# Kernel optimization log

Measured on AMD Instinct MI355X. Metric: run time of the kernel, lower is better.

The kernel has to match this reference:

```python
import jax, jax.numpy as jnp
import numpy as np

DIM = 384
HEADS = 8


def setup_inputs() -> dict:
    key = jax.random.key(0)
    ks = jax.random.split(key, 8)
    d = DIM
    return {
        "x": jax.random.normal(ks[0], (4, d, 128, 128), jnp.float32),
        "message": jax.random.normal(ks[1], (4, d, 128, 128), jnp.float32),
        "temperature": jnp.ones((HEADS, 1, 1), jnp.float32),
        "qkv_w": jax.random.normal(ks[2], (3 * d, d), jnp.float32) * 0.02,   # 1x1 conv weight
        "dw_w": jax.random.normal(ks[3], (3 * d, 1, 3, 3), jnp.float32) * 0.02,  # depthwise 3x3
        "proj_w": jax.random.normal(ks[4], (d, d), jnp.float32) * 0.02,     # project_out 1x1
        "lin_w": jax.random.normal(ks[5], (d, 2 * d), jnp.float32) * 0.02,  # nn.Linear weight [out,in]
        "lin_b": jnp.zeros((d,), jnp.float32),
    }


def _qkv_branch(t, qkv_w, dw_w):
    # 1x1 conv (pointwise) then depthwise 3x3, groups = 3*dim
    y = jnp.einsum('oc,bchw->bohw', qkv_w, t)
    y = jax.lax.conv_general_dilated(
        y, dw_w, window_strides=(1, 1), padding='SAME',
        dimension_numbers=('NCHW', 'OIHW', 'NCHW'),
        feature_group_count=dw_w.shape[0])
    return jnp.split(y, 3, axis=1)  # q, k, v each [b, dim, h, w]


def _to_heads(t):
    b, c, h, w = t.shape
    return t.reshape(b, HEADS, c // HEADS, h * w)  # [b, head, c, n]


def _l2norm(t):
    # torch F.normalize(dim=-1, eps=1e-12)
    n = jnp.sqrt(jnp.sum(t * t, axis=-1, keepdims=True))
    return t / jnp.maximum(n, 1e-12)


def reference(x, message, temperature, qkv_w, dw_w, proj_w, lin_w, lin_b):
    b, c, h, w = x.shape
    q, k, v = (_to_heads(t) for t in _qkv_branch(x, qkv_w, dw_w))
    q_m, k_m, v_m = (_to_heads(t) for t in _qkv_branch(message, qkv_w, dw_w))

    k_c = jnp.concatenate([k, k_m], axis=2)   # [b, head, 2c, n]
    v_c = jnp.concatenate([v, v_m], axis=2)

    q = _l2norm(q)
    k_c = _l2norm(k_c)
    q_m = _l2norm(q_m)

    # channel attention: [b, head, c, 2c]
    attn1 = jax.nn.softmax(jnp.einsum('bhcn,bhdn->bhcd', q, k_c) * temperature, axis=-1)
    attn2 = jax.nn.softmax(jnp.einsum('bhcn,bhdn->bhcd', q_m, k_c) * temperature, axis=-1)

    out1 = jnp.einsum('bhcd,bhdn->bhcn', attn1, v_c)  # [b, head, c, n]
    out2 = jnp.einsum('bhcd,bhdn->bhcn', attn2, v_c)

    # 'b head c (h w) -> b (h w) (head c)'
    out1 = out1.transpose(0, 3, 1, 2).reshape(b, h * w, c)
    out2 = out2.transpose(0, 3, 1, 2).reshape(b, h * w, c)

    cat = jnp.concatenate([out1, out2], axis=2)  # [b, n, 2c]
    out = cat @ lin_w.T + lin_b                  # [b, n, c]

    # 'b (h w) c -> b c h w'
    out = out.transpose(0, 2, 1).reshape(b, c, h, w)
    out = jnp.einsum('oc,bchw->bohw', proj_w, out)
    return out
```

## Files before the change

kernel.cpp:

```cpp
#include <hip/hip_runtime.h>

typedef unsigned short u16;
typedef unsigned int u32;

#define BATCH 4
#define CDIM 384
#define IMG 128
#define HW 16384
#define QKVC 1152
#define NHEADS 8
#define CHD 48
#define DD2 96
#define KFIN 768

typedef __attribute__((ext_vector_type(8))) short bf16x8;
typedef __attribute__((ext_vector_type(4))) float f32x4;

__device__ __forceinline__ u16 f2bf(float f){
  union { float f; u32 u; } v; v.f = f;
  u32 u = v.u;
  u32 r = (u + 0x7fffu + ((u >> 16) & 1u)) >> 16;
  return (u16)r;
}
__device__ __forceinline__ float bf2f(u16 h){
  union { u32 u; float f; } v; v.u = ((u32)h) << 16;
  return v.f;
}

#define OFF_QKVX  ((size_t)0)
#define OFF_QKVM  ((size_t)150994944)
#define OFF_T     ((size_t)301989888)
#define OFF_SSQ   ((size_t)339738624)
#define OFF_S     ((size_t)339775488)
#define OFF_ATTN  ((size_t)340955136)
#define OFF_AFINB ((size_t)342134784)
#define OFF_W2    ((size_t)344494080)
#define OFF_B2    ((size_t)345673728)
#define OFF_WB    ((size_t)345675264)

typedef __attribute__((address_space(1))) const u32 gas_u32;
typedef __attribute__((address_space(3))) u32 las_u32;
__device__ __forceinline__ void gl_lds16(const u16* g, u16* l){
  __builtin_amdgcn_global_load_lds((gas_u32*)g, (las_u32*)l, 16, 0, 0);
}

__device__ __forceinline__ u16* t_row(u16* T0, u16* qkvm, int par, int ch){
  if (par == 0) return T0 + (size_t)ch * HW;
  int bq = ch / 384;
  int rr = ch - bq * 384;
  return qkvm + ((size_t)bq * QKVC + 2 * CDIM + rr) * HW;
}

__global__ void __launch_bounds__(256) k_w2(const float* __restrict__ proj,
                                            const float* __restrict__ lin,
                                            const float* __restrict__ linb,
                                            const float* __restrict__ qkvw,
                                            float* __restrict__ W2,
                                            float* __restrict__ b2,
                                            u16* __restrict__ Wb){
  int idx = blockIdx.x * 256 + threadIdx.x;
  if (idx < CDIM * KFIN){
    int o = idx / KFIN, d = idx % KFIN;
    float acc = 0.f;
    for (int c = 0; c < CDIM; c++)
      acc = fmaf(proj[o * CDIM + c], lin[c * KFIN + d], acc);
    W2[idx] = acc;
  }
  if (idx < CDIM){
    float acc = 0.f;
    for (int c = 0; c < CDIM; c++)
      acc = fmaf(proj[idx * CDIM + c], linb[c], acc);
    b2[idx] = acc;
  }
  if (idx < QKVC * CDIM) Wb[idx] = f2bf(qkvw[idx]);
}

__device__ __forceinline__ void loadrow(const u16* __restrict__ src, int r, int cg, float* o){
  if ((unsigned)r >= IMG){
    #pragma unroll
    for (int i = 0; i < 18; i++) o[i] = 0.f;
    return;
  }
  const u16* p = src + (size_t)r * IMG + cg * 16;
  uint4 v0 = *(const uint4*)p;
  uint4 v1 = *(const uint4*)(p + 8);
  u32 ww[8] = {v0.x, v0.y, v0.z, v0.w, v1.x, v1.y, v1.z, v1.w};
  #pragma unroll
  for (int i = 0; i < 8; i++){
    union { u32 u; float f; } lo, hi;
    lo.u = ww[i] << 16;
    hi.u = ww[i] & 0xffff0000u;
    o[1 + 2 * i] = lo.f;
    o[2 + 2 * i] = hi.f;
  }
  o[0]  = (cg > 0) ? bf2f(p[-1]) : 0.f;
  o[17] = (cg < 7) ? bf2f(p[16]) : 0.f;
}

#define LCHUNK 1024
__global__ void __launch_bounds__(256) k_stage(
    int t, int npw, int nlog, int ndw, int ncvt,
    const u16* __restrict__ Wb, u16* __restrict__ Bt,
    u16* __restrict__ T0, u16* __restrict__ qkvx, u16* __restrict__ qkvm,
    const float* __restrict__ x, const float* __restrict__ msg,
    const float* __restrict__ dww, float* __restrict__ ssq,
    float* __restrict__ S){
  __shared__ __align__(16) u16 smem[16384];
  int bid = blockIdx.x;
  int tid = threadIdx.x;

  if (bid < npw){
    int z = t - 1, par = z & 1;
    const u16* B = Bt + (size_t)z * HW * CDIM;
    u16* As = smem;
    u16* Bs = smem + 8192;
    int swz = (bid & 7) * 144 + (bid >> 3);
    int bx = swz % 9, by = swz / 9;
    int m0 = bx * 128, n0 = by * 128;
    int w = tid >> 6, lane = tid & 63;
    int wy = w >> 1, wx = w & 1;
    int lm = lane & 15, q = lane >> 4;

    int srow = w * 16 + (lane >> 2);
    int scol = (lane & 3) * 8;
    const u16* ga = Wb + (size_t)(m0 + srow) * CDIM + scol;
    const u16* gb = B + (size_t)(n0 + srow) * CDIM + scol;
    u16* la = As + srow * 32 + scol;
    u16* lb = Bs + srow * 32 + scol;

    f32x4 acc[4][4];
    #pragma unroll
    for (int i = 0; i < 4; i++)
      #pragma unroll
      for (int j = 0; j < 4; j++) acc[i][j] = (f32x4){0.f,0.f,0.f,0.f};

#define PW_STAGE(buf, k0) do{ \
      gl_lds16(ga + (k0),             la + (buf) * 4096); \
      gl_lds16(ga + 64*CDIM + (k0),   la + (buf) * 4096 + 2048); \
      gl_lds16(gb + (k0),             lb + (buf) * 4096); \
      gl_lds16(gb + 64*CDIM + (k0),   lb + (buf) * 4096 + 2048); \
    }while(0)

    PW_STAGE(0, 0);
    __syncthreads();
    int cur = 0;
    for (int kt = 0; kt < 12; kt++){
      if (kt < 11) PW_STAGE(cur ^ 1, (kt + 1) * 32);
      bf16x8 af[4], bfr[4];
      #pragma unroll
      for (int i = 0; i < 4; i++)
        af[i] = *(const bf16x8*)&As[cur * 4096 + (wy * 64 + i * 16 + lm) * 32 + q * 8];
      #pragma unroll
      for (int j = 0; j < 4; j++)
        bfr[j] = *(const bf16x8*)&Bs[cur * 4096 + (wx * 64 + j * 16 + lm) * 32 + q * 8];
      #pragma unroll
      for (int i = 0; i < 4; i++)
        #pragma unroll
        for (int j = 0; j < 4; j++)
          acc[i][j] = __builtin_amdgcn_mfma_f32_16x16x32_bf16(af[i], bfr[j], acc[i][j], 0, 0, 0);
      __syncthreads();
      cur ^= 1;
    }
#undef PW_STAGE
    #pragma unroll
    for (int i = 0; i < 4; i++){
      #pragma unroll
      for (int r = 0; r < 4; r++){
        int row = m0 + wy * 64 + i * 16 + q * 4 + r;
        u16* cp = t_row(T0, qkvm, par, row) + n0 + wx * 64 + lm;
        #pragma unroll
        for (int j = 0; j < 4; j++)
          cp[j * 16] = f2bf(acc[i][j][r]);
      }
    }

  } else if (bid < npw + nlog){
    int idx = bid - npw;
    int b = t - 7;
    int nc = idx & 15;
    int h = idx >> 4;
    int w = tid >> 6, lane = tid & 63;
    int wy = w >> 1, wx = w & 1;
    int lm = lane & 15, quad = lane >> 4;

    const u16* ap[3]; const u16* bp[3];
    #pragma unroll
    for (int i = 0; i < 3; i++){
      int g = wy * 48 + i * 16 + lm;
      int c = (g < 48) ? g : g - 48;
      ap[i] = ((g < 48) ? qkvx : qkvm) + ((size_t)b * QKVC + h * CHD + c) * HW;
      int d = wx * 48 + i * 16 + lm;
      int cc = (d < 48) ? d : d - 48;
      bp[i] = ((d < 48) ? qkvx : qkvm) + ((size_t)b * QKVC + CDIM + h * CHD + cc) * HW;
    }
    f32x4 acc[3][3];
    #pragma unroll
    for (int i = 0; i < 3; i++)
      #pragma unroll
      for (int j = 0; j < 3; j++) acc[i][j] = (f32x4){0.f,0.f,0.f,0.f};

    int nbeg = nc * LCHUNK + quad * 8;
    int nend = nc * LCHUNK + LCHUNK;
    for (int n = nbeg; n < nend; n += 32){
      bf16x8 af[3], bfr[3];
      #pragma unroll
      for (int i = 0; i < 3; i++) af[i]  = *(const bf16x8*)(ap[i] + n);
      #pragma unroll
      for (int j = 0; j < 3; j++) bfr[j] = *(const bf16x8*)(bp[j] + n);
      #pragma unroll
      for (int i = 0; i < 3; i++)
        #pragma unroll
        for (int j = 0; j < 3; j++)
          acc[i][j] = __builtin_amdgcn_mfma_f32_16x16x32_bf16(af[i], bfr[j], acc[i][j], 0, 0, 0);
    }
    #pragma unroll
    for (int i = 0; i < 3; i++){
      #pragma unroll
      for (int r = 0; r < 4; r++){
        int g = wy * 48 + i * 16 + quad * 4 + r;
        int iq = (g >= 48) ? 1 : 0;
        int c = iq ? g - 48 : g;
        float* Sp = S + (((size_t)(iq * BATCH + b) * NHEADS + h) * CHD + c) * DD2;
        #pragma unroll
        for (int j = 0; j < 3; j++)
          atomicAdd(&Sp[wx * 48 + j * 16 + lm], acc[i][j][r]);
      }
    }

  } else if (bid < npw + nlog + ndw){
    int ch = bid - npw - nlog;
    int z = t - 2, par = z & 1;
    const u16* src = t_row(T0, qkvm, par, ch);
    u16* dst;
    if (ch < 2 * CDIM){
      u16* qd = ((z >> 2) ? qkvm : qkvx) + (size_t)(z & 3) * QKVC * HW;
      dst = qd + (size_t)ch * HW;
    } else {
      dst = Bt + (size_t)z * HW * CDIM + (size_t)(ch - 2 * CDIM) * HW;
    }
    float w[9];
    #pragma unroll
    for (int t9 = 0; t9 < 9; t9++) w[t9] = dww[ch * 9 + t9];
    int rg = tid >> 3, cg = tid & 7;
    int r0 = rg * 4;
    float ra[18], rb[18], rc[18];
    loadrow(src, r0 - 1, cg, ra);
    loadrow(src, r0,     cg, rb);
    float ss = 0.f;
    #pragma unroll
    for (int rr = 0; rr < 4; rr++){
      int r = r0 + rr;
      loadrow(src, r + 1, cg, rc);
      u32 pk[8];
      #pragma unroll
      for (int xx = 0; xx < 16; xx++){
        float a2 = w[0] * ra[xx];
        a2 = fmaf(w[1], ra[xx + 1], a2);
        a2 = fmaf(w[2], ra[xx + 2], a2);
        a2 = fmaf(w[3], rb[xx],     a2);
        a2 = fmaf(w[4], rb[xx + 1], a2);
        a2 = fmaf(w[5], rb[xx + 2], a2);
        a2 = fmaf(w[6], rc[xx],     a2);
        a2 = fmaf(w[7], rc[xx + 1], a2);
        a2 = fmaf(w[8], rc[xx + 2], a2);
        ss = fmaf(a2, a2, ss);
        u16 hv = f2bf(a2);
        if (xx & 1) pk[xx >> 1] |= (u32)hv << 16;
        else        pk[xx >> 1]  = (u32)hv;
      }
      *(uint4*)(dst + (size_t)r * IMG + cg * 16)     = *(uint4*)&pk[0];
      *(uint4*)(dst + (size_t)r * IMG + cg * 16 + 8) = *(uint4*)&pk[4];
      #pragma unroll
      for (int ii = 0; ii < 18; ii++){ ra[ii] = rb[ii]; rb[ii] = rc[ii]; }
    }
    if (ch < 2 * CDIM){
      float* red = (float*)smem;
      red[tid] = ss;
      __syncthreads();
      for (int s = 128; s > 0; s >>= 1){
        if (tid < s) red[tid] += red[tid + s];
        __syncthreads();
      }
      if (tid == 0) ssq[(size_t)z * QKVC + ch] = red[0];
    }

  } else if (bid < npw + nlog + ndw + ncvt){
    int cb = bid - npw - nlog - ndw;
    int z = t;
    const float* src = (z < 4 ? x : msg) + (size_t)(z & 3) * CDIM * HW;
    u16* dstz = Bt + (size_t)z * HW * CDIM;
    int n0 = (cb & 127) * 128;
    int c0 = (cb >> 7) * 64;
    u16 (*tile)[130] = (u16(*)[130])smem;
    #pragma unroll
    for (int i = 0; i < 8; i++){
      int c = (tid >> 5) + i * 8;
      int nq = tid & 31;
      float4 v = *(const float4*)(src + (size_t)(c0 + c) * HW + n0 + nq * 4);
      u32 p0 = (u32)f2bf(v.x) | ((u32)f2bf(v.y) << 16);
      u32 p1 = (u32)f2bf(v.z) | ((u32)f2bf(v.w) << 16);
      *(u32*)&tile[c][nq * 4]     = p0;
      *(u32*)&tile[c][nq * 4 + 2] = p1;
    }
    __syncthreads();
    #pragma unroll
    for (int u = 0; u < 2; u++){
      int idx = tid + u * 256;
      int n = idx >> 2, j = idx & 3;
      u32 pk[8];
      #pragma unroll
      for (int p = 0; p < 8; p++)
        pk[p] = (u32)tile[j * 16 + 2 * p][n] | ((u32)tile[j * 16 + 2 * p + 1][n] << 16);
      u16* dp = dstz + (size_t)(n0 + n) * CDIM + c0 + j * 16;
      *(uint4*)dp       = *(uint4*)&pk[0];
      *(uint4*)(dp + 8) = *(uint4*)&pk[4];
    }

  } else {
    int v = bid - npw - nlog - ndw - ncvt;
    int z, h, nb;
    if (v < 512){ z = t - 3; h = v >> 7; nb = v & 127; }
    else { int u = v - 512; z = u >> 9; h = 4 + ((u >> 7) & 3); nb = u & 127; }
    int inp = z >> 2, b = z & 3;
    const u16* vcn = Bt + (size_t)z * HW * CDIM;
    int n0 = nb * 128;
    u16* vt = (h < 4 ? qkvx : qkvm) + ((size_t)b * QKVC + 2 * CDIM) * HW;
    int dbase = (h & 3) * 96 + inp * 48;
    u16 (*tile)[136] = (u16(*)[136])smem;
    #pragma unroll
    for (int j = 0; j < 3; j++){
      int i = tid + j * 256;
      int row = i >> 4, c8 = i & 15;
      uint4 vv = *(const uint4*)(vcn + (size_t)(h * 48 + row) * HW + n0 + c8 * 8);
      *(uint4*)&tile[row][c8 * 8] = vv;
    }
    __syncthreads();
    #pragma unroll
    for (int pass = 0; pass < 3; pass++){
      int idx = tid + pass * 256;
      int n = idx / 6, part = idx - n * 6;
      u32 pk[4];
      #pragma unroll
      for (int p = 0; p < 4; p++){
        int c = part * 8 + p * 2;
        pk[p] = (u32)tile[c][n] | ((u32)tile[c + 1][n] << 16);
      }
      *(uint4*)(vt + (size_t)(n0 + n) * CDIM + dbase + part * 8) = *(uint4*)pk;
    }
  }
}

__global__ void __launch_bounds__(128) k_softmax(const float* __restrict__ S,
                                                 const float* __restrict__ ssq,
                                                 const float* __restrict__ temp,
                                                 float* __restrict__ attn){
  int row = blockIdx.x;
  int c = row % CHD;
  int h = (row / CHD) % NHEADS;
  int b = (row / (CHD * NHEADS)) % BATCH;
  int iq = row / (CHD * NHEADS * BATCH);
  int tid = threadIdx.x;
  __shared__ float sh[128];
  const float* Sp = S + (size_t)row * DD2;
  float ssq_q = ssq[(iq * BATCH + b) * QKVC + h * CHD + c];
  float nq = fmaxf(sqrtf(ssq_q), 1e-12f);
  float tmp = temp[h];
  float logit = -1e30f;
  int d = tid;
  if (d < DD2){
    float ssq_k = ssq[((d < CHD ? 0 : 1) * BATCH + b) * QKVC + CDIM + h * CHD + (d % CHD)];
    float nk = fmaxf(sqrtf(ssq_k), 1e-12f);
    logit = Sp[d] * tmp / (nq * nk);
  }
  sh[tid] = logit; __syncthreads();
  for (int s = 64; s > 0; s >>= 1){
    if (tid < s) sh[tid] = fmaxf(sh[tid], sh[tid + s]);
    __syncthreads();
  }
  float mx = sh[0]; __syncthreads();
  float e = (d < DD2) ? expf(logit - mx) : 0.f;
  sh[tid] = e; __syncthreads();
  for (int s = 64; s > 0; s >>= 1){
    if (tid < s) sh[tid] += sh[tid + s];
    __syncthreads();
  }
  float sum = sh[0];
  if (d < DD2) attn[(size_t)row * DD2 + d] = e / sum;
}

__global__ void __launch_bounds__(128) k_mmat(const float* __restrict__ attn,
                                              const float* __restrict__ W2,
                                              u16* __restrict__ AfinB){
  int oz = blockIdx.x;
  int h = blockIdx.y;
  int b = blockIdx.z;
  __shared__ float a1[CHD * DD2];
  __shared__ float a2[CHD * DD2];
  int tid = threadIdx.x;
  const float* A1 = attn + ((size_t)(0 * BATCH + b) * NHEADS + h) * CHD * DD2;
  const float* A2 = attn + ((size_t)(1 * BATCH + b) * NHEADS + h) * CHD * DD2;
  for (int i = tid; i < CHD * DD2; i += 128){ a1[i] = A1[i]; a2[i] = A2[i]; }
  __syncthreads();
  int e = tid;
  if (e < DD2){
    for (int oo = 0; oo < 8; oo++){
      int o = oz * 8 + oo;
      float acc = 0.f;
      #pragma unroll 4
      for (int cc = 0; cc < CHD; cc++){
        acc = fmaf(W2[o * KFIN + h * CHD + cc],        a1[cc * DD2 + e], acc);
        acc = fmaf(W2[o * KFIN + CDIM + h * CHD + cc], a2[cc * DD2 + e], acc);
      }
      AfinB[((size_t)b * CDIM + o) * KFIN + h * DD2 + e] = f2bf(acc);
    }
  }
}

__global__ void __launch_bounds__(256) k_fin(const u16* __restrict__ AfB,
                                             const u16* __restrict__ qkvx,
                                             const u16* __restrict__ qkvm,
                                             const float* __restrict__ b2,
                                             float* __restrict__ out){
  __shared__ __align__(16) u16 As[2 * 4096];
  __shared__ __align__(16) u16 Bs[2 * 4096];
  int orig = blockIdx.x;
  int swz = (orig & 7) * 192 + (orig >> 3);
  int m = swz % 3;
  int rest = swz / 3;
  int n0 = (rest & 127) * 128;
  int bz = rest >> 7;
  int m0 = m * 128;
  int tid = threadIdx.x;
  int w = tid >> 6, lane = tid & 63;
  int wy = w >> 1, wx = w & 1;
  int lm = lane & 15, q = lane >> 4;

  int srow = w * 16 + (lane >> 2);
  int scol = (lane & 3) * 8;
  const u16* A = AfB + (size_t)bz * CDIM * KFIN;
  const u16* ga  = A + (size_t)(m0 + srow) * KFIN + scol;
  const u16* gb0 = qkvx + ((size_t)bz * QKVC + 2 * CDIM) * HW + (size_t)(n0 + srow) * CDIM + scol;
  const u16* gb1 = qkvm + ((size_t)bz * QKVC + 2 * CDIM) * HW + (size_t)(n0 + srow) * CDIM + scol;
  u16* la = As + srow * 32 + scol;
  u16* lb = Bs + srow * 32 + scol;

  f32x4 acc[4][4];
  #pragma unroll
  for (int i = 0; i < 4; i++)
    #pragma unroll
    for (int j = 0; j < 4; j++) acc[i][j] = (f32x4){0.f,0.f,0.f,0.f};

#define FIN_STAGE(buf, t) do{ \
    int hp_ = (t) >= 12; \
    int k0_ = ((t) - hp_ * 12) * 32; \
    const u16* gb_ = hp_ ? gb1 : gb0; \
    gl_lds16(ga + hp_ * CDIM + k0_,            la + (buf) * 4096); \
    gl_lds16(ga + hp_ * CDIM + k0_ + 64*KFIN,  la + (buf) * 4096 + 2048); \
    gl_lds16(gb_ + k0_,                        lb + (buf) * 4096); \
    gl_lds16(gb_ + k0_ + 64*CDIM,              lb + (buf) * 4096 + 2048); \
  }while(0)

  FIN_STAGE(0, 0);
  __syncthreads();
  int cur = 0;
  for (int t = 0; t < 24; t++){
    if (t < 23) FIN_STAGE(cur ^ 1, t + 1);
    bf16x8 af[4], bfr[4];
    #pragma unroll
    for (int i = 0; i < 4; i++)
      af[i] = *(const bf16x8*)&As[cur * 4096 + (wy * 64 + i * 16 + lm) * 32 + q * 8];
    #pragma unroll
    for (int j = 0; j < 4; j++)
      bfr[j] = *(const bf16x8*)&Bs[cur * 4096 + (wx * 64 + j * 16 + lm) * 32 + q * 8];
    #pragma unroll
    for (int i = 0; i < 4; i++)
      #pragma unroll
      for (int j = 0; j < 4; j++)
        acc[i][j] = __builtin_amdgcn_mfma_f32_16x16x32_bf16(af[i], bfr[j], acc[i][j], 0, 0, 0);
    __syncthreads();
    cur ^= 1;
  }
#undef FIN_STAGE
  #pragma unroll
  for (int i = 0; i < 4; i++){
    #pragma unroll
    for (int r = 0; r < 4; r++){
      int row = m0 + wy * 64 + i * 16 + q * 4 + r;
      float bv = b2[row];
      float* cp = out + (size_t)bz * CDIM * HW + (size_t)row * HW + n0 + wx * 64 + lm;
      #pragma unroll
      for (int j = 0; j < 4; j++)
        cp[j * 16] = acc[i][j][r] + bv;
    }
  }
}

extern "C" void kernel_launch(void* const* d_in, const int* in_sizes, int n_in,
                              void* d_out, int out_size, void* d_ws, size_t ws_size,
                              hipStream_t stream){
  const float* x      = (const float*)d_in[0];
  const float* msg    = (const float*)d_in[1];
  const float* temp   = (const float*)d_in[2];
  const float* qkv_w  = (const float*)d_in[3];
  const float* dw_w   = (const float*)d_in[4];
  const float* proj_w = (const float*)d_in[5];
  const float* lin_w  = (const float*)d_in[6];
  const float* lin_b  = (const float*)d_in[7];
  float* out = (float*)d_out;

  char* ws = (char*)d_ws;
  u16*   qkvx  = (u16*)(ws + OFF_QKVX);
  u16*   qkvm  = (u16*)(ws + OFF_QKVM);
  u16*   T0    = (u16*)(ws + OFF_T);
  float* ssq   = (float*)(ws + OFF_SSQ);
  float* S     = (float*)(ws + OFF_S);
  float* attn  = (float*)(ws + OFF_ATTN);
  u16*   AfinB = (u16*)(ws + OFF_AFINB);
  float* W2    = (float*)(ws + OFF_W2);
  float* b2    = (float*)(ws + OFF_B2);
  u16*   Wb    = (u16*)(ws + OFF_WB);

  u16* Bt = (u16*)d_out;

  hipMemsetAsync(ws + OFF_S, 0, (OFF_ATTN - OFF_S), stream);

  k_w2<<<dim3((QKVC * CDIM + 255) / 256), dim3(256), 0, stream>>>(
      proj_w, lin_w, lin_b, qkv_w, W2, b2, Wb);

  for (int t = 0; t < 11; t++){
    int npw  = (t >= 1 && t <= 8) ? 1152 : 0;
    int ndw  = (t >= 2 && t <= 9) ? 1152 : 0;
    int ncvt = (t <= 7) ? 768 : 0;
    int nlog = (t >= 7) ? 128 : 0;
    int nvt  = (t >= 3) ? ((t == 10) ? 4608 : 512) : 0;
    k_stage<<<dim3(npw + nlog + ndw + ncvt + nvt), dim3(256), 0, stream>>>(
        t, npw, nlog, ndw, ncvt, Wb, Bt, T0, qkvx, qkvm, x, msg, dw_w, ssq, S);
  }

  k_softmax<<<dim3(2 * BATCH * NHEADS * CHD), dim3(128), 0, stream>>>(S, ssq, temp, attn);
  k_mmat<<<dim3(CDIM / 8, NHEADS, BATCH), dim3(128), 0, stream>>>(attn, W2, AfinB);
  k_fin<<<dim3(3 * (HW / 128) * BATCH), dim3(256), 0, stream>>>(
      AfinB, qkvx, qkvm, b2, out);
}
```

Before: 881.4 us.

## Interleave stage roles across grid and rebalance logit chunks and V-transpose work

```diff
diff --git a/kernel.cpp b/kernel.cpp
--- a/kernel.cpp
+++ b/kernel.cpp
@@ -97,9 +97,9 @@
   o[17] = (cg < 7) ? bf2f(p[16]) : 0.f;
 }
 
-#define LCHUNK 1024
+#define LCHUNK 512
 __global__ void __launch_bounds__(256) k_stage(
-    int t, int npw, int nlog, int ndw, int ncvt,
+    int t, int npw, int nlog, int ndw, int ncvt, int nvt,
     const u16* __restrict__ Wb, u16* __restrict__ Bt,
     u16* __restrict__ T0, u16* __restrict__ qkvx, u16* __restrict__ qkvm,
     const float* __restrict__ x, const float* __restrict__ msg,
@@ -109,12 +109,25 @@
   int bid = blockIdx.x;
   int tid = threadIdx.x;
 
-  if (bid < npw){
+  int role, ridx;
+  if (bid < nlog){ role = 1; ridx = bid; }
+  else {
+    int rb = bid - nlog;
+    int cpw = npw >> 4, cdw = ndw >> 4, ccv = ncvt >> 4, cvv = nvt >> 4;
+    int per = cpw + cdw + ccv + cvv;
+    int g = rb / per, o = rb - g * per;
+    if (o < cpw){ role = 0; ridx = g * cpw + o; }
+    else if (o < cpw + cdw){ role = 2; ridx = g * cdw + (o - cpw); }
+    else if (o < cpw + cdw + ccv){ role = 3; ridx = g * ccv + (o - cpw - cdw); }
+    else { role = 4; ridx = g * cvv + (o - cpw - cdw - ccv); }
+  }
+
+  if (role == 0){
     int z = t - 1, par = z & 1;
     const u16* B = Bt + (size_t)z * HW * CDIM;
     u16* As = smem;
     u16* Bs = smem + 8192;
-    int swz = (bid & 7) * 144 + (bid >> 3);
+    int swz = (ridx & 7) * 144 + (ridx >> 3);
     int bx = swz % 9, by = swz / 9;
     int m0 = bx * 128, n0 = by * 128;
     int w = tid >> 6, lane = tid & 63;
@@ -174,11 +187,10 @@
       }
     }
 
-  } else if (bid < npw + nlog){
-    int idx = bid - npw;
+  } else if (role == 1){
     int b = t - 7;
-    int nc = idx & 15;
-    int h = idx >> 4;
+    int nc = ridx & 31;
+    int h = ridx >> 5;
     int w = tid >> 6, lane = tid & 63;
     int wy = w >> 1, wx = w & 1;
     int lm = lane & 15, quad = lane >> 4;
@@ -227,8 +239,8 @@
       }
     }
 
-  } else if (bid < npw + nlog + ndw){
-    int ch = bid - npw - nlog;
+  } else if (role == 2){
+    int ch = ridx;
     int z = t - 2, par = z & 1;
     const u16* src = t_row(T0, qkvm, par, ch);
     u16* dst;
@@ -284,8 +296,8 @@
       if (tid == 0) ssq[(size_t)z * QKVC + ch] = red[0];
     }
 
-  } else if (bid < npw + nlog + ndw + ncvt){
-    int cb = bid - npw - nlog - ndw;
+  } else if (role == 3){
+    int cb = ridx;
     int z = t;
     const float* src = (z < 4 ? x : msg) + (size_t)(z & 3) * CDIM * HW;
     u16* dstz = Bt + (size_t)z * HW * CDIM;
@@ -317,10 +329,11 @@
     }
 
   } else {
-    int v = bid - npw - nlog - ndw - ncvt;
+    int iv = ridx;
     int z, h, nb;
-    if (v < 512){ z = t - 3; h = v >> 7; nb = v & 127; }
-    else { int u = v - 512; z = u >> 9; h = 4 + ((u >> 7) & 3); nb = u & 127; }
+    if (iv < 512){ z = t - 3; h = iv >> 7; nb = iv & 127; }
+    else if (t == 6){ int u = iv - 512; z = 3; h = 4 + ((u >> 7) & 3); nb = u & 127; }
+    else { int u = iv - 512; int zz = u >> 9; z = (zz < 3) ? zz : zz + 1; h = 4 + ((u >> 7) & 3); nb = u & 127; }
     int inp = z >> 2, b = z & 3;
     const u16* vcn = Bt + (size_t)z * HW * CDIM;
     int n0 = nb * 128;
@@ -527,14 +540,17 @@
   k_w2<<<dim3((QKVC * CDIM + 255) / 256), dim3(256), 0, stream>>>(
       proj_w, lin_w, lin_b, qkv_w, W2, b2, Wb);
 
-  for (int t = 0; t < 11; t++){
+  for (int t = 0; t <= 10; t++){
     int npw  = (t >= 1 && t <= 8) ? 1152 : 0;
     int ndw  = (t >= 2 && t <= 9) ? 1152 : 0;
     int ncvt = (t <= 7) ? 768 : 0;
-    int nlog = (t >= 7) ? 128 : 0;
-    int nvt  = (t >= 3) ? ((t == 10) ? 4608 : 512) : 0;
-    k_stage<<<dim3(npw + nlog + ndw + ncvt + nvt), dim3(256), 0, stream>>>(
-        t, npw, nlog, ndw, ncvt, Wb, Bt, T0, qkvx, qkvm, x, msg, dw_w, ssq, S);
+    int nlog = (t >= 7) ? 256 : 0;
+    int nvt  = 0;
+    if (t >= 3 && t <= 9) nvt = 512;
+    if (t == 6) nvt = 1024;
+    if (t == 10) nvt = 512 + 3584;
+    k_stage<<<dim3(nlog + npw + ndw + ncvt + nvt), dim3(256), 0, stream>>>(
+        t, npw, nlog, ndw, ncvt, nvt, Wb, Bt, T0, qkvx, qkvm, x, msg, dw_w, ssq, S);
   }
 
   k_softmax<<<dim3(2 * BATCH * NHEADS * CHD), dim3(128), 0, stream>>>(S, ssq, temp, attn);
```

New measurement: 867.2 us. Within noise of the previous version (-1.6%).
